# Optimization experiments

Measured on AMD Instinct MI355X. Metric: run time of the kernel, lower is better.

Reference implementation:

```python
import jax, jax.numpy as jnp
import numpy as np

B, SD, SE = 4, 2048, 2048
HID, HID_ = 300, 512
N_HEADS = 8


def setup_inputs() -> dict:
    key = jax.random.key(0)
    ks = jax.random.split(key, 7)
    en = jax.random.normal(ks[0], (B, SE, HID), dtype=jnp.float32)
    de = jax.random.normal(ks[1], (B, SD, HID), dtype=jnp.float32)
    mask = jax.random.randint(ks[2], (1, 1, SD, SE), 0, 2).astype(jnp.bool_)
    WQ = jax.random.normal(ks[3], (HID, HID_), dtype=jnp.float32)
    WK = jax.random.normal(ks[4], (HID, HID_), dtype=jnp.float32)
    WV = jax.random.normal(ks[5], (HID, HID_), dtype=jnp.float32)
    WO = jax.random.normal(ks[6], (HID_, HID), dtype=jnp.float32)
    return {"en": en, "de": de, "mask": mask, "WQ": WQ, "WK": WK, "WV": WV, "WO": WO}


def reference(en, de, mask, WQ, WK, WV, WO):
    # Faithful to the torch module (dropout in eval mode => identity).
    d_k = de.shape[-1]  # NOTE: original scales by sqrt(hidden_dim)=sqrt(300), not head_dim
    b_d, s_d = de.shape[0], de.shape[1]
    b_e, s_e = en.shape[0], en.shape[1]
    # head axis is the LAST axis of the reshape (size 8), exactly as the original view/permute
    q = jnp.transpose((de @ WQ).reshape(b_d, s_d, -1, N_HEADS), (3, 0, 1, 2))  # [8,B,Sd,64]
    k = jnp.transpose((en @ WK).reshape(b_e, s_e, -1, N_HEADS), (3, 0, 2, 1))  # [8,B,64,Se]
    v = jnp.transpose((en @ WV).reshape(b_e, s_e, -1, N_HEADS), (3, 0, 1, 2))  # [8,B,Se,64]
    e = jnp.matmul(q, k) / jnp.sqrt(jnp.asarray(d_k, dtype=q.dtype))           # [8,B,Sd,Se]
    e = jnp.where(mask, jnp.asarray(-1e9, dtype=e.dtype), e)
    alpha = jax.nn.softmax(e, axis=3)
    head3 = jnp.matmul(alpha, v)                                               # [8,B,Sd,64]
    # torch.cat((head3[0],...,head3[7]), 2) == move head axis into feature concat order
    a = jnp.concatenate([head3[h] for h in range(N_HEADS)], axis=2)            # [B,Sd,512]
    return a @ WO                                                              # [B,Sd,300]
```

## Files before the change

### kernel.cpp

```cpp
#include <hip/hip_runtime.h>
#include <hip/hip_bf16.h>
#include <math.h>

#define B_      4
#define SD_     2048
#define SE_     2048
#define HIDIN   300
#define HIDMID  512
#define NH      8
#define DH      64
#define ESZ     ((size_t)4194304)
#define BUFB    24576

typedef __attribute__((ext_vector_type(8))) short          s16x8;
typedef __attribute__((ext_vector_type(8))) unsigned short u16x8;
typedef __attribute__((ext_vector_type(4))) unsigned short u16x4;
typedef __attribute__((ext_vector_type(4))) float          f32x4;

#define MFMA16 __builtin_amdgcn_mfma_f32_16x16x32_bf16

#define QSCALE  0.0832940411f
#define NEGL   -1.4426950e9f
#define DEFER_THR 24.0f

__device__ __forceinline__ unsigned short f2bf(float f) {
    unsigned int u = __float_as_uint(f);
    u += 0x7fffu + ((u >> 16) & 1u);
    return (unsigned short)(u >> 16);
}
__device__ __forceinline__ float bf2f(unsigned short s) {
    return __uint_as_float((unsigned int)s << 16);
}
__device__ __forceinline__ void gload16(const void* g, void* l) {
    __builtin_amdgcn_global_load_lds(
        (const __attribute__((address_space(1))) void*)g,
        (__attribute__((address_space(3))) void*)l, 16, 0, 0);
}
__device__ __forceinline__ float fexp2(float x) {
#if __has_builtin(__builtin_amdgcn_exp2f)
    return __builtin_amdgcn_exp2f(x);
#else
    return exp2f(x);
#endif
}

#define OF_QH   ((size_t)0)
#define OF_QL   (ESZ)
#define OF_KH   (2*ESZ)
#define OF_KL   (3*ESZ)
#define OF_VT   (4*ESZ)
#define OF_CA   (5*ESZ)
#define OF_CW   (OF_CA + 10485760)
#define OF_WOT  (OF_CW + 983040)

__global__ __launch_bounds__(256) void bias_kernel(const int* __restrict__ mask,
                                                   unsigned int* __restrict__ BiasT)
{
    const int idx = blockIdx.x * 256 + threadIdx.x;
    const int q = idx >> 5, tile = idx & 31;
    const int* __restrict__ mrow = mask + (size_t)q * SE_ + tile * 64;
    const unsigned int NEGB = (unsigned int)f2bf(NEGL);
    const int qblk = q >> 4, qlo = q & 15;
#pragma unroll
    for (int g = 0; g < 4; ++g) {
        unsigned int w[8];
#pragma unroll
        for (int sub = 0; sub < 4; ++sub) {
            const int4 mm = *(const int4*)(mrow + sub * 16 + g * 4);
            w[sub * 2]     = (mm.x ? NEGB : 0u) | ((mm.y ? NEGB : 0u) << 16);
            w[sub * 2 + 1] = (mm.z ? NEGB : 0u) | ((mm.w ? NEGB : 0u) << 16);
        }
        unsigned int* dst = BiasT +
            ((((size_t)qblk * 32 + tile) * 4 + g) * 16 + qlo) * 8;
        *(uint4*)dst       = make_uint4(w[0], w[1], w[2], w[3]);
        *(uint4*)(dst + 4) = make_uint4(w[4], w[5], w[6], w[7]);
    }
}

__global__ __launch_bounds__(256) void convA_kernel(
    const float* __restrict__ de, const float* __restrict__ en,
    unsigned short* __restrict__ CA)
{
    const int idx = blockIdx.x * 256 + threadIdx.x;
    const int mat = blockIdx.y;
    const float* __restrict__ A = mat ? en : de;
    unsigned short* __restrict__ H = CA + (size_t)mat * 5242880;
    unsigned short* __restrict__ L = H + 2621440;
    const int row = idx / 10, ch = idx - row * 10;
    float v[32];
    if (ch < 9) {
#pragma unroll
        for (int i = 0; i < 8; ++i) {
            const float4 f = *(const float4*)(A + (size_t)row * 300 + ch * 32 + i * 4);
            v[i*4+0] = f.x; v[i*4+1] = f.y; v[i*4+2] = f.z; v[i*4+3] = f.w;
        }
    } else {
#pragma unroll
        for (int i = 0; i < 32; ++i) {
            const int k = 288 + i;
            v[i] = (k < 300) ? A[(size_t)row * 300 + k] : 0.f;
        }
    }
    const int r128 = row & 127;
    const int xr = (r128 >> 1) & 3;
    const size_t tb = ((size_t)(row >> 7) * 10 + ch) * 4096 + r128 * 32;
#pragma unroll
    for (int sub = 0; sub < 4; ++sub) {
        const int slot = sub ^ xr;
        u16x8 hv, lv;
#pragma unroll
        for (int e = 0; e < 8; ++e) {
            const float f = v[sub * 8 + e];
            const unsigned short h = f2bf(f);
            hv[e] = h; lv[e] = f2bf(f - bf2f(h));
        }
        *(u16x8*)(H + tb + slot * 8) = hv;
        *(u16x8*)(L + tb + slot * 8) = lv;
    }
}

__global__ __launch_bounds__(256) void convW_kernel(
    const float* __restrict__ WQ, const float* __restrict__ WK,
    const float* __restrict__ WV, const float* __restrict__ WO,
    unsigned short* __restrict__ CW, unsigned short* __restrict__ WOT)
{
    const int idx = blockIdx.x * 256 + threadIdx.x;
    if (idx < 122880) {
        const int which = idx / 40960;
        const int rem = idx - which * 40960;
        const int k = rem >> 7;
        const int n0 = (rem & 127) * 4;
        const float* __restrict__ W = which == 0 ? WQ : (which == 1 ? WK : WV);
        unsigned short* __restrict__ H = CW + (size_t)which * 327680;
        unsigned short* __restrict__ L = H + 163840;
        const float sc = (which == 0) ? QSCALE : 1.f;
        float4 w = make_float4(0.f, 0.f, 0.f, 0.f);
        if (k < 300) w = *(const float4*)(W + (size_t)k * 512 + n0);
        const float wv4[4] = {w.x * sc, w.y * sc, w.z * sc, w.w * sc};
        const int ch = k >> 5, kk = k & 31;
#pragma unroll
        for (int j = 0; j < 4; ++j) {
            const int n = n0 + j, ntile = n >> 7, nr = n & 127;
            const size_t o = ((size_t)(ntile * 10 + ch) * 128 + nr) * 32
                           + (((kk >> 3) ^ ((nr >> 1) & 3)) << 3) + (kk & 7);
            const unsigned short h = f2bf(wv4[j]);
            H[o] = h;
            if (which < 2) L[o] = f2bf(wv4[j] - bf2f(h));
        }
    } else {
        const int idx2 = idx - 122880;
        const int k = idx2 / 96, n4 = idx2 - k * 96;
        const int n0 = n4 * 4;
        float4 w = make_float4(0.f, 0.f, 0.f, 0.f);
        if (n0 < 300) w = *(const float4*)(WO + (size_t)k * 300 + n0);
        const float wv4[4] = {w.x, w.y, w.z, w.w};
        const int ch = k >> 5, kk = k & 31;
#pragma unroll
        for (int j = 0; j < 4; ++j) {
            const int n = n0 + j, ntile = n >> 7, nr = n & 127;
            const size_t o = ((size_t)(ntile * 16 + ch) * 128 + nr) * 32
                           + (((kk >> 3) ^ ((nr >> 1) & 3)) << 3) + (kk & 7);
            WOT[o] = f2bf(wv4[j]);
        }
    }
}

__global__ __launch_bounds__(256) void proj_qk_kernel(
    const unsigned short* __restrict__ CA, const unsigned short* __restrict__ CW,
    unsigned short* __restrict__ Qh, unsigned short* __restrict__ Ql,
    unsigned short* __restrict__ KhT, unsigned short* __restrict__ KlT)
{
    const int lin = blockIdx.x;
    const int which = lin >> 8;
    const int t = lin & 255;
    const int stile = (t & 7) | ((t >> 5) << 3);
    const int jtile = (t >> 3) & 3;
    const int tid = threadIdx.x, wv = tid >> 6, lane = tid & 63;
    const int li = lane & 15, g = lane >> 4;
    const int wr = wv >> 1, wc = wv & 1;

    __shared__ __align__(16) char LBp[65536];

    const unsigned short* __restrict__ pAh =
        CA + (size_t)which * 5242880 + (size_t)stile * 40960 + tid * 8;
    const unsigned short* __restrict__ pAl = pAh + 2621440;
    const unsigned short* __restrict__ pWh =
        CW + (size_t)which * 327680 + (size_t)jtile * 40960 + tid * 8;
    const unsigned short* __restrict__ pWl = pWh + 163840;

#define STAGEP(ch, bofs) {                                                    \
        char* db = LBp + (bofs) + wv * 1024;                                  \
        const size_t co = (size_t)(ch) * 4096;                                \
        gload16(pAh + co,        db);                                         \
        gload16(pAh + co + 2048, db + 4096);                                  \
        gload16(pAl + co,        db + 8192);                                  \
        gload16(pAl + co + 2048, db + 12288);                                 \
        gload16(pWh + co,        db + 16384);                                 \
        gload16(pWh + co + 2048, db + 20480);                                 \
        gload16(pWl + co,        db + 24576);                                 \
        gload16(pWl + co + 2048, db + 28672);                                 \
    }

    int offA[4], offW[4];
#pragma unroll
    for (int ssub = 0; ssub < 4; ++ssub) {
        const int r = wr * 64 + ssub * 16 + li;
        offA[ssub] = r * 64 + ((g ^ ((r >> 1) & 3)) << 4);
    }
#pragma unroll
    for (int jsub = 0; jsub < 4; ++jsub) {
        const int n = wc * 64 + jsub * 16 + li;
        offW[jsub] = n * 64 + ((g ^ ((n >> 1) & 3)) << 4);
    }

    f32x4 acc[4][4];
#pragma unroll
    for (int i = 0; i < 4; ++i)
#pragma unroll
        for (int j = 0; j < 4; ++j) acc[i][j] = (f32x4){0.f, 0.f, 0.f, 0.f};

    STAGEP(0, 0)
    __syncthreads();

#pragma unroll 1
    for (int ch = 0; ch < 10; ++ch) {
        const int bofs = (ch & 1) * 32768;
        if (ch < 9) STAGEP(ch + 1, bofs ^ 32768)
        const char* bp = LBp + bofs;
        s16x8 ah[4], al[4], wh[4], wl[4];
#pragma unroll
        for (int ssub = 0; ssub < 4; ++ssub) {
            ah[ssub] = *(const s16x8*)(bp + offA[ssub]);
            al[ssub] = *(const s16x8*)(bp + 8192 + offA[ssub]);
        }
#pragma unroll
        for (int jsub = 0; jsub < 4; ++jsub) {
            wh[jsub] = *(const s16x8*)(bp + 16384 + offW[jsub]);
            wl[jsub] = *(const s16x8*)(bp + 24576 + offW[jsub]);
        }
        __builtin_amdgcn_s_setprio(1);
#pragma unroll
        for (int ssub = 0; ssub < 4; ++ssub)
#pragma unroll
            for (int jsub = 0; jsub < 4; ++jsub) {
                acc[ssub][jsub] = MFMA16(ah[ssub], wh[jsub], acc[ssub][jsub], 0, 0, 0);
                acc[ssub][jsub] = MFMA16(ah[ssub], wl[jsub], acc[ssub][jsub], 0, 0, 0);
                acc[ssub][jsub] = MFMA16(al[ssub], wh[jsub], acc[ssub][jsub], 0, 0, 0);
            }
        __builtin_amdgcn_s_setprio(0);
        __syncthreads();
    }
#undef STAGEP

    const int jgbase = jtile * 128 + wc * 64 + li;
    const int sbase0 = stile * 128 + wr * 64 + 4 * g;
#pragma unroll
    for (int jsub = 0; jsub < 4; ++jsub) {
        const int jgg = jgbase + jsub * 16;
        const int d = jgg >> 3, hh = jgg & 7;
#pragma unroll
        for (int ssub = 0; ssub < 4; ++ssub) {
            const f32x4 v = acc[ssub][jsub];
            const int sg0 = sbase0 + ssub * 16;
            const int bbv = sg0 >> 11;
            const int bhn = bbv * 8 + hh;
            const int sl0 = sg0 & 2047;
            if (which == 0) {
                const size_t o = ((size_t)bhn * 2048 + sl0) * 64 + d;
#pragma unroll
                for (int r = 0; r < 4; ++r) {
                    const float val = v[r];
                    const unsigned short hi = f2bf(val);
                    Qh[o + r * 64] = hi;
                    Ql[o + r * 64] = f2bf(val - bf2f(hi));
                }
            } else {
                const int tile = sl0 >> 6, tt0 = sl0 & 63;
                const size_t tb = ((size_t)(bhn * 32 + tile)) << 12;
#pragma unroll
                for (int r = 0; r < 4; ++r) {
                    const int tt = tt0 + r;
                    const size_t o = tb + tt * 64 + (((d >> 3) ^ (tt & 7)) << 3) + (d & 7);
                    const float val = v[r];
                    const unsigned short hi = f2bf(val);
                    KhT[o] = hi;
                    KlT[o] = f2bf(val - bf2f(hi));
                }
            }
        }
    }
}

__global__ __launch_bounds__(256) void proj_v_kernel(
    const unsigned short* __restrict__ CA, const unsigned short* __restrict__ CW,
    unsigned short* __restrict__ VtT)
{
    const int t = blockIdx.x;
    const int stile = (t & 7) | ((t >> 5) << 3);
    const int jtile = (t >> 3) & 3;
    const int tid = threadIdx.x, wv = tid >> 6, lane = tid & 63;
    const int li = lane & 15, g = lane >> 4;
    const int wr = wv >> 1, wc = wv & 1;

    __shared__ __align__(16) char LBv[32768];

    const unsigned short* __restrict__ pAh =
        CA + (size_t)1 * 5242880 + (size_t)stile * 40960 + tid * 8;
    const unsigned short* __restrict__ pWh =
        CW + (size_t)2 * 327680 + (size_t)jtile * 40960 + tid * 8;

#define STAGEV(ch, bofs) {                                                    \
        char* db = LBv + (bofs) + wv * 1024;                                  \
        const size_t co = (size_t)(ch) * 4096;                                \
        gload16(pAh + co,        db);                                         \
        gload16(pAh + co + 2048, db + 4096);                                  \
        gload16(pWh + co,        db + 8192);                                  \
        gload16(pWh + co + 2048, db + 12288);                                 \
    }

    int offA[4], offW[4];
#pragma unroll
    for (int ssub = 0; ssub < 4; ++ssub) {
        const int r = wr * 64 + ssub * 16 + li;
        offA[ssub] = r * 64 + ((g ^ ((r >> 1) & 3)) << 4);
    }
#pragma unroll
    for (int jsub = 0; jsub < 4; ++jsub) {
        const int n = wc * 64 + jsub * 16 + li;
        offW[jsub] = 8192 + n * 64 + ((g ^ ((n >> 1) & 3)) << 4);
    }

    f32x4 acc[4][4];
#pragma unroll
    for (int i = 0; i < 4; ++i)
#pragma unroll
        for (int j = 0; j < 4; ++j) acc[i][j] = (f32x4){0.f, 0.f, 0.f, 0.f};

    STAGEV(0, 0)
    __syncthreads();

#pragma unroll 1
    for (int ch = 0; ch < 10; ++ch) {
        const int bofs = (ch & 1) * 16384;
        if (ch < 9) STAGEV(ch + 1, bofs ^ 16384)
        const char* bp = LBv + bofs;
        s16x8 ah[4], wh[4];
#pragma unroll
        for (int ssub = 0; ssub < 4; ++ssub)
            ah[ssub] = *(const s16x8*)(bp + offA[ssub]);
#pragma unroll
        for (int jsub = 0; jsub < 4; ++jsub)
            wh[jsub] = *(const s16x8*)(bp + offW[jsub]);
        __builtin_amdgcn_s_setprio(1);
#pragma unroll
        for (int ssub = 0; ssub < 4; ++ssub)
#pragma unroll
            for (int jsub = 0; jsub < 4; ++jsub)
                acc[ssub][jsub] = MFMA16(ah[ssub], wh[jsub], acc[ssub][jsub], 0, 0, 0);
        __builtin_amdgcn_s_setprio(0);
        __syncthreads();
    }
#undef STAGEV

    const int jgbase = jtile * 128 + wc * 64 + li;
    const int sbase0 = stile * 128 + wr * 64 + 4 * g;
#pragma unroll
    for (int jsub = 0; jsub < 4; ++jsub) {
        const int jgg = jgbase + jsub * 16;
        const int d = jgg >> 3, hh = jgg & 7;
#pragma unroll
        for (int ssub = 0; ssub < 4; ++ssub) {
            const f32x4 v = acc[ssub][jsub];
            const int sg0 = sbase0 + ssub * 16;
            const int bbv = sg0 >> 11;
            const int bhn = bbv * 8 + hh;
            const int sl0 = sg0 & 2047;
            const int tile = sl0 >> 6, tin0 = sl0 & 63;
            const size_t tb = ((size_t)(bhn * 32 + tile)) << 12;
            const int blk = tin0 >> 5, gg2 = (tin0 >> 2) & 3, half = (tin0 >> 4) & 1;
            const size_t o = tb + (size_t)d * 64
                           + ((((blk << 2) | gg2) ^ (d & 7)) << 3) + half * 4;
            u16x4 pk;
#pragma unroll
            for (int r = 0; r < 4; ++r) pk[r] = f2bf(v[r]);
            *(u16x4*)(VtT + o) = pk;
        }
    }
}

__global__ __launch_bounds__(512, 4) void attn_mfma_kernel(
    const unsigned short* __restrict__ Qh, const unsigned short* __restrict__ Ql,
    const unsigned short* __restrict__ KhT, const unsigned short* __restrict__ KlT,
    const unsigned short* __restrict__ VtT, const unsigned int* __restrict__ BiasT,
    unsigned short* __restrict__ AOb)
{
    const int lin = blockIdx.x + 16 * blockIdx.y;
    const int qt = (lin >> 3) & 15;
    const int bh = (lin & 7) + ((lin >> 7) << 3);
    const int bb = bh >> 3, hh = bh & 7;
    const int tid = threadIdx.x;
    const int wv = tid >> 6, lane = tid & 63;
    const int g = lane >> 4, li = lane & 15;
    const int q = qt * 128 + wv * 16 + li;

    __shared__ __align__(16) char LB[3 * BUFB];

    const size_t qoff = ((size_t)bh * SD_ + q) * DH + 8 * g;
    const s16x8 qh0 = *(const s16x8*)(Qh + qoff);
    const s16x8 qh1 = *(const s16x8*)(Qh + qoff + 32);
    const s16x8 ql0 = *(const s16x8*)(Ql + qoff);
    const s16x8 ql1 = *(const s16x8*)(Ql + qoff + 32);

    const unsigned short* __restrict__ sKh = KhT + ((size_t)bh << 17) + tid * 8;
    const unsigned short* __restrict__ sKl = KlT + ((size_t)bh << 17) + tid * 8;
    const unsigned short* __restrict__ sVt = VtT + ((size_t)bh << 17) + tid * 8;

    const int base0 = li * 128 + ((g ^ (li & 7)) << 4);
    const int base1 = li * 128 + (((4 + g) ^ (li & 7)) << 4);

    const size_t bbase = (size_t)(qt * 8 + wv) * 16384 + g * 128 + li * 8;

#define BIASLOAD(T, RA, RB) {                                                 \
        const uint4* p = (const uint4*)(BiasT + bbase + (size_t)(T) * 512);   \
        RA = p[0]; RB = p[1];                                                 \
    }
#define STAGE(tile, boff)                                                     \
    {                                                                         \
        char* db = LB + (boff) + wv * 1024;                                   \
        const size_t toff = (size_t)(tile) << 12;                             \
        gload16(sKh + toff, db);                                              \
        gload16(sKl + toff, db + 8192);                                       \
        gload16(sVt + toff, db + 16384);                                      \
    }

    float m = -INFINITY;
    f32x4 O[4], lacc;
#pragma unroll
    for (int i = 0; i < 4; ++i) O[i] = (f32x4){0.f, 0.f, 0.f, 0.f};
    lacc = (f32x4){0.f, 0.f, 0.f, 0.f};

    s16x8 ones;
#pragma unroll
    for (int i = 0; i < 8; ++i) ones[i] = (short)0x3F80;

    uint4 cBA, cBB, nBA, nBB;

#define UNPK(W, S, sub, cbase)                                                \
        S[sub][cbase]     = __uint_as_float((W) << 16);                       \
        S[sub][cbase + 1] = __uint_as_float((W) & 0xFFFF0000u);

#define ITER(IT, CBA_, CBB_, NBA_, NBB_)                                      \
    {                                                                         \
        BIASLOAD(((IT) + 1) & 31, NBA_, NBB_)                                 \
        STAGE(((IT) + 2) & 31, cs)                                            \
        f32x4 s[4];                                                           \
        UNPK(CBA_.x, s, 0, 0) UNPK(CBA_.y, s, 0, 2)                           \
        UNPK(CBA_.z, s, 1, 0) UNPK(CBA_.w, s, 1, 2)                           \
        UNPK(CBB_.x, s, 2, 0) UNPK(CBB_.y, s, 2, 2)                           \
        UNPK(CBB_.z, s, 3, 0) UNPK(CBB_.w, s, 3, 2)                           \
        __builtin_amdgcn_s_setprio(1);                                        \
        _Pragma("unroll")                                                     \
        for (int sub = 0; sub < 4; ++sub) {                                   \
            const s16x8 kh0 = *(const s16x8*)(LB + cc + base0 + sub * 2048);  \
            const s16x8 kh1 = *(const s16x8*)(LB + cc + base1 + sub * 2048);  \
            const s16x8 kl0 = *(const s16x8*)(LB + cc + base0 + 8192 + sub * 2048); \
            const s16x8 kl1 = *(const s16x8*)(LB + cc + base1 + 8192 + sub * 2048); \
            s[sub] = MFMA16(kh0, qh0, s[sub], 0, 0, 0);                       \
            s[sub] = MFMA16(kh0, ql0, s[sub], 0, 0, 0);                       \
            s[sub] = MFMA16(kl0, qh0, s[sub], 0, 0, 0);                       \
            s[sub] = MFMA16(kh1, qh1, s[sub], 0, 0, 0);                       \
            s[sub] = MFMA16(kh1, ql1, s[sub], 0, 0, 0);                       \
            s[sub] = MFMA16(kl1, qh1, s[sub], 0, 0, 0);                       \
        }                                                                     \
        __builtin_amdgcn_s_setprio(0);                                        \
        float x0 = fmaxf(fmaxf(s[0][0], s[0][1]), s[0][2]);                   \
        float x1 = fmaxf(fmaxf(s[0][3], s[1][0]), s[1][1]);                   \
        float x2 = fmaxf(fmaxf(s[1][2], s[1][3]), s[2][0]);                   \
        float x3 = fmaxf(fmaxf(s[2][1], s[2][2]), s[2][3]);                   \
        float x4 = fmaxf(fmaxf(s[3][0], s[3][1]), s[3][2]);                   \
        float tmax = fmaxf(fmaxf(fmaxf(x0, x1), fmaxf(x2, x3)),               \
                           fmaxf(x4, s[3][3]));                               \
        if (!__all(tmax <= m + DEFER_THR)) {                                  \
            float r = fmaxf(tmax, __shfl_xor(tmax, 16));                      \
            r = fmaxf(r, __shfl_xor(r, 32));                                  \
            const float mn  = fmaxf(m, r);                                    \
            const float scl = fexp2(m - mn);                                  \
            m = mn;                                                           \
            _Pragma("unroll")                                                 \
            for (int i = 0; i < 4; ++i) O[i] *= scl;                          \
            lacc *= scl;                                                      \
        }                                                                     \
        _Pragma("unroll")                                                     \
        for (int sub = 0; sub < 4; ++sub)                                     \
            _Pragma("unroll")                                                 \
            for (int c = 0; c < 4; ++c)                                       \
                s[sub][c] = fexp2(s[sub][c] - m);                             \
        union { s16x8 v; unsigned int w[4]; } P0, P1;                         \
        asm("v_cvt_pk_bf16_f32 %0, %1, %2" : "=v"(P0.w[0]) : "v"(s[0][0]), "v"(s[0][1])); \
        asm("v_cvt_pk_bf16_f32 %0, %1, %2" : "=v"(P0.w[1]) : "v"(s[0][2]), "v"(s[0][3])); \
        asm("v_cvt_pk_bf16_f32 %0, %1, %2" : "=v"(P0.w[2]) : "v"(s[1][0]), "v"(s[1][1])); \
        asm("v_cvt_pk_bf16_f32 %0, %1, %2" : "=v"(P0.w[3]) : "v"(s[1][2]), "v"(s[1][3])); \
        asm("v_cvt_pk_bf16_f32 %0, %1, %2" : "=v"(P1.w[0]) : "v"(s[2][0]), "v"(s[2][1])); \
        asm("v_cvt_pk_bf16_f32 %0, %1, %2" : "=v"(P1.w[1]) : "v"(s[2][2]), "v"(s[2][3])); \
        asm("v_cvt_pk_bf16_f32 %0, %1, %2" : "=v"(P1.w[2]) : "v"(s[3][0]), "v"(s[3][1])); \
        asm("v_cvt_pk_bf16_f32 %0, %1, %2" : "=v"(P1.w[3]) : "v"(s[3][2]), "v"(s[3][3])); \
        __builtin_amdgcn_s_setprio(1);                                        \
        _Pragma("unroll")                                                     \
        for (int dsub = 0; dsub < 4; ++dsub) {                                \
            const s16x8 vf0 = *(const s16x8*)(LB + cc + base0 + 16384 + dsub * 2048); \
            const s16x8 vf1 = *(const s16x8*)(LB + cc + base1 + 16384 + dsub * 2048); \
            O[dsub] = MFMA16(vf0, P0.v, O[dsub], 0, 0, 0);                    \
            O[dsub] = MFMA16(vf1, P1.v, O[dsub], 0, 0, 0);                    \
        }                                                                     \
        lacc = MFMA16(ones, P0.v, lacc, 0, 0, 0);                             \
        lacc = MFMA16(ones, P1.v, lacc, 0, 0, 0);                             \
        __builtin_amdgcn_s_setprio(0);                                        \
        asm volatile("s_waitcnt vmcnt(3)" ::: "memory");                      \
        __builtin_amdgcn_s_barrier();                                         \
        __builtin_amdgcn_sched_barrier(0);                                    \
        cc += BUFB; if (cc == 3 * BUFB) cc = 0;                               \
        cs += BUFB; if (cs == 3 * BUFB) cs = 0;                               \
    }

    int cc = 0, cs = 2 * BUFB;

    BIASLOAD(0, cBA, cBB)
    STAGE(0, 0)
    STAGE(1, BUFB)
    asm volatile("s_waitcnt vmcnt(3)" ::: "memory");
    __builtin_amdgcn_s_barrier();
    __builtin_amdgcn_sched_barrier(0);

#pragma unroll 1
    for (int it = 0; it < 32; it += 2) {
        ITER(it,     cBA, cBB, nBA, nBB)
        ITER(it + 1, nBA, nBB, cBA, cBB)
    }

    const float rl = 1.f / lacc[0];
    const int row = bb * 2048 + q;
    const int r128 = row & 127;
    const int xr = (r128 >> 1) & 3;
    unsigned short* __restrict__ ab = AOb + ((size_t)(row >> 7)) * 65536
                                    + r128 * 32 + (g & 1) * 4;
#pragma unroll
    for (int dsub = 0; dsub < 4; ++dsub) {
        const f32x4 o = O[dsub] * rl;
        const int ch = hh * 2 + (dsub >> 1);
        const int slot = ((dsub & 1) * 2 + (g >> 1)) ^ xr;
        u16x4 pk;
#pragma unroll
        for (int c = 0; c < 4; ++c) pk[c] = f2bf(o[c]);
        *(u16x4*)(ab + (size_t)ch * 4096 + slot * 8) = pk;
    }
#undef STAGE
#undef BIASLOAD
#undef UNPK
#undef ITER
}

__global__ __launch_bounds__(256) void epi_mfma_kernel(
    const unsigned short* __restrict__ AOb, const unsigned short* __restrict__ WOT,
    float* __restrict__ out)
{
    const int stile = blockIdx.x, jtile = blockIdx.y;
    const int tid = threadIdx.x, wv = tid >> 6, lane = tid & 63;
    const int li = lane & 15, g = lane >> 4;

    __shared__ __align__(16) char LBe[24576];

    const unsigned short* __restrict__ pA =
        AOb + (size_t)(stile >> 1) * 65536 + (stile & 1) * 2048 + tid * 8;
    const unsigned short* __restrict__ pW = WOT + (size_t)jtile * 65536 + tid * 8;

#define STAGEE(ch, bofs) {                                                    \
        char* dbA = LBe + (bofs) + wv * 1024;                                 \
        const size_t co = (size_t)(ch) * 4096;                                \
        gload16(pA + co,        dbA);                                         \
        gload16(pW + co,        dbA + 4096);                                  \
        gload16(pW + co + 2048, dbA + 8192);                                  \
    }

    int offA[4], offW[2];
#pragma unroll
    for (int ssub = 0; ssub < 4; ++ssub) {
        const int r = ssub * 16 + li;
        offA[ssub] = r * 64 + ((g ^ ((r >> 1) & 3)) << 4);
    }
#pragma unroll
    for (int jsub = 0; jsub < 2; ++jsub) {
        const int n = wv * 32 + jsub * 16 + li;
        offW[jsub] = 4096 + n * 64 + ((g ^ ((n >> 1) & 3)) << 4);
    }

    f32x4 acc[4][2];
#pragma unroll
    for (int i = 0; i < 4; ++i)
#pragma unroll
        for (int j = 0; j < 2; ++j) acc[i][j] = (f32x4){0.f, 0.f, 0.f, 0.f};

    STAGEE(0, 0)
    __syncthreads();

#pragma unroll 1
    for (int ch = 0; ch < 16; ++ch) {
        const int bofs = (ch & 1) * 12288;
        if (ch < 15) STAGEE(ch + 1, bofs ^ 12288)
        const char* bp = LBe + bofs;
        s16x8 ah[4], wh[2];
#pragma unroll
        for (int ssub = 0; ssub < 4; ++ssub)
            ah[ssub] = *(const s16x8*)(bp + offA[ssub]);
#pragma unroll
        for (int jsub = 0; jsub < 2; ++jsub)
            wh[jsub] = *(const s16x8*)(bp + offW[jsub]);
        __builtin_amdgcn_s_setprio(1);
#pragma unroll
        for (int ssub = 0; ssub < 4; ++ssub)
#pragma unroll
            for (int jsub = 0; jsub < 2; ++jsub)
                acc[ssub][jsub] = MFMA16(ah[ssub], wh[jsub], acc[ssub][jsub], 0, 0, 0);
        __builtin_amdgcn_s_setprio(0);
        __syncthreads();
    }
#undef STAGEE

    const int nbase = jtile * 128 + wv * 32 + li;
    const int rbase = stile * 64 + 4 * g;
#pragma unroll
    for (int jsub = 0; jsub < 2; ++jsub) {
        const int o = nbase + jsub * 16;
        if (o < HIDIN) {
#pragma unroll
            for (int ssub = 0; ssub < 4; ++ssub) {
                const f32x4 v = acc[ssub][jsub];
                const int r0 = rbase + ssub * 16;
#pragma unroll
                for (int r = 0; r < 4; ++r)
                    out[(size_t)(r0 + r) * HIDIN + o] = v[r];
            }
        }
    }
}

extern "C" void kernel_launch(void* const* d_in, const int* in_sizes, int n_in,
                              void* d_out, int out_size, void* d_ws, size_t ws_size,
                              hipStream_t stream)
{
    const float* en  = (const float*)d_in[0];
    const float* de  = (const float*)d_in[1];
    const int*   mask = (const int*)d_in[2];
    const float* WQ  = (const float*)d_in[3];
    const float* WK  = (const float*)d_in[4];
    const float* WV  = (const float*)d_in[5];
    const float* WO  = (const float*)d_in[6];
    float* out = (float*)d_out;

    unsigned short* ws2 = (unsigned short*)d_ws;
    unsigned short* Qh  = ws2 + OF_QH;
    unsigned short* Ql  = ws2 + OF_QL;
    unsigned short* KhT = ws2 + OF_KH;
    unsigned short* KlT = ws2 + OF_KL;
    unsigned short* VtT = ws2 + OF_VT;
    unsigned short* CA  = ws2 + OF_CA;
    unsigned short* CW  = ws2 + OF_CW;
    unsigned short* WOT = ws2 + OF_WOT;
    unsigned short* AOb = CA;
    unsigned int*  BiasT = (unsigned int*)(CA + 4194304);

    convA_kernel<<<dim3(320, 2), 256, 0, stream>>>(de, en, CA);
    convW_kernel<<<dim3(672), 256, 0, stream>>>(WQ, WK, WV, WO, CW, WOT);
    proj_qk_kernel<<<dim3(512), 256, 0, stream>>>(CA, CW, Qh, Ql, KhT, KlT);
    proj_v_kernel<<<dim3(256), 256, 0, stream>>>(CA, CW, VtT);
    bias_kernel<<<dim3(256), 256, 0, stream>>>(mask, BiasT);
    attn_mfma_kernel<<<dim3(16, 32), 512, 0, stream>>>(Qh, Ql, KhT, KlT, VtT,
                                                       BiasT, AOb);
    epi_mfma_kernel<<<dim3(128, 3), 256, 0, stream>>>(AOb, WOT, out);
}
```

Before: 176.0 us.

## Switch attention kernel to 32x32x16 MFMA tiles with 4-wave blocks

Rewrites the attention kernel to use 32x32x16 bf16 MFMA instructions instead of 16x16x32. Each wave now handles 32 query rows, and blocks shrink from 8 to 4 waves. The bias and V-transpose layouts are rearranged to match the new accumulator fragment layout. The row sum, previously computed with an MFMA against a ones vector, is now a VALU tree reduction. The aim is to cut LDS fragment reads per FLOP and MFMA issue overhead, at the cost of more registers per wave and fewer waves per CU.

```diff
diff --git a/kernel.cpp b/kernel.cpp
--- a/kernel.cpp
+++ b/kernel.cpp
@@ -12,12 +12,14 @@
 #define ESZ     ((size_t)4194304)
 #define BUFB    24576
 
-typedef __attribute__((ext_vector_type(8))) short          s16x8;
-typedef __attribute__((ext_vector_type(8))) unsigned short u16x8;
-typedef __attribute__((ext_vector_type(4))) unsigned short u16x4;
-typedef __attribute__((ext_vector_type(4))) float          f32x4;
+typedef __attribute__((ext_vector_type(8)))  short          s16x8;
+typedef __attribute__((ext_vector_type(8)))  unsigned short u16x8;
+typedef __attribute__((ext_vector_type(4)))  unsigned short u16x4;
+typedef __attribute__((ext_vector_type(4)))  float          f32x4;
+typedef __attribute__((ext_vector_type(16))) float          f32x16;
 
 #define MFMA16 __builtin_amdgcn_mfma_f32_16x16x32_bf16
+#define MFMA32 __builtin_amdgcn_mfma_f32_32x32x16_bf16
 
 #define QSCALE  0.0832940411f
 #define NEGL   -1.4426950e9f
@@ -57,23 +59,31 @@
                                                    unsigned int* __restrict__ BiasT)
 {
     const int idx = blockIdx.x * 256 + threadIdx.x;
-    const int q = idx >> 5, tile = idx & 31;
-    const int* __restrict__ mrow = mask + (size_t)q * SE_ + tile * 64;
+    const int q = idx >> 5, t64 = idx & 31;
+    const int* __restrict__ mrow = mask + (size_t)q * SE_ + t64 * 64;
     const unsigned int NEGB = (unsigned int)f2bf(NEGL);
-    const int qblk = q >> 4, qlo = q & 15;
-#pragma unroll
-    for (int g = 0; g < 4; ++g) {
-        unsigned int w[8];
-#pragma unroll
-        for (int sub = 0; sub < 4; ++sub) {
-            const int4 mm = *(const int4*)(mrow + sub * 16 + g * 4);
-            w[sub * 2]     = (mm.x ? NEGB : 0u) | ((mm.y ? NEGB : 0u) << 16);
-            w[sub * 2 + 1] = (mm.z ? NEGB : 0u) | ((mm.w ? NEGB : 0u) << 16);
-        }
-        unsigned int* dst = BiasT +
-            ((((size_t)qblk * 32 + tile) * 4 + g) * 16 + qlo) * 8;
-        *(uint4*)dst       = make_uint4(w[0], w[1], w[2], w[3]);
-        *(uint4*)(dst + 4) = make_uint4(w[4], w[5], w[6], w[7]);
+    int mv[64];
+#pragma unroll
+    for (int i = 0; i < 16; ++i) {
+        const int4 mm = *(const int4*)(mrow + i * 4);
+        mv[i*4+0] = mm.x; mv[i*4+1] = mm.y; mv[i*4+2] = mm.z; mv[i*4+3] = mm.w;
+    }
+    uint4* __restrict__ dst4 = (uint4*)BiasT;
+    const size_t cbase = ((size_t)(q >> 5) * 32 + t64) * 4;
+#pragma unroll
+    for (int hi = 0; hi < 2; ++hi) {
+#pragma unroll
+        for (int L = 0; L < 4; ++L) {
+            unsigned int wd[4];
+#pragma unroll
+            for (int i = 0; i < 4; ++i) {
+                const int w = L * 4 + i;
+                const int t0 = (w >> 3) * 32 + 2 * (w & 1) + 8 * ((w & 7) >> 1) + 4 * hi;
+                wd[i] = (mv[t0] ? NEGB : 0u) | ((mv[t0 + 1] ? NEGB : 0u) << 16);
+            }
+            dst4[(cbase + L) * 64 + hi * 32 + (q & 31)] =
+                make_uint4(wd[0], wd[1], wd[2], wd[3]);
+        }
     }
 }
 
@@ -377,9 +387,9 @@
             const int sl0 = sg0 & 2047;
             const int tile = sl0 >> 6, tin0 = sl0 & 63;
             const size_t tb = ((size_t)(bhn * 32 + tile)) << 12;
-            const int blk = tin0 >> 5, gg2 = (tin0 >> 2) & 3, half = (tin0 >> 4) & 1;
-            const size_t o = tb + (size_t)d * 64
-                           + ((((blk << 2) | gg2) ^ (d & 7)) << 3) + half * 4;
+            const int s_pre = ((tin0 >> 4) << 1) | ((tin0 >> 2) & 1);
+            const int j0 = ((tin0 >> 3) & 1) * 4;
+            const size_t o = tb + (size_t)d * 64 + ((s_pre ^ (d & 7)) << 3) + j0;
             u16x4 pk;
 #pragma unroll
             for (int r = 0; r < 4; ++r) pk[r] = f2bf(v[r]);
@@ -388,7 +398,7 @@
     }
 }
 
-__global__ __launch_bounds__(512, 4) void attn_mfma_kernel(
+__global__ __launch_bounds__(256, 2) void attn32_kernel(
     const unsigned short* __restrict__ Qh, const unsigned short* __restrict__ Ql,
     const unsigned short* __restrict__ KhT, const unsigned short* __restrict__ KlT,
     const unsigned short* __restrict__ VtT, const unsigned int* __restrict__ BiasT,
@@ -400,122 +410,156 @@
     const int bb = bh >> 3, hh = bh & 7;
     const int tid = threadIdx.x;
     const int wv = tid >> 6, lane = tid & 63;
-    const int g = lane >> 4, li = lane & 15;
-    const int q = qt * 128 + wv * 16 + li;
+    const int hi = lane >> 5, l31 = lane & 31, l7 = lane & 7;
+    const int q = qt * 128 + wv * 32 + l31;
 
     __shared__ __align__(16) char LB[3 * BUFB];
 
-    const size_t qoff = ((size_t)bh * SD_ + q) * DH + 8 * g;
-    const s16x8 qh0 = *(const s16x8*)(Qh + qoff);
-    const s16x8 qh1 = *(const s16x8*)(Qh + qoff + 32);
-    const s16x8 ql0 = *(const s16x8*)(Ql + qoff);
-    const s16x8 ql1 = *(const s16x8*)(Ql + qoff + 32);
+    const size_t qoff = ((size_t)bh * SD_ + q) * DH + hi * 8;
+    s16x8 qh[4], ql[4];
+#pragma unroll
+    for (int c = 0; c < 4; ++c) {
+        qh[c] = *(const s16x8*)(Qh + qoff + c * 16);
+        ql[c] = *(const s16x8*)(Ql + qoff + c * 16);
+    }
 
     const unsigned short* __restrict__ sKh = KhT + ((size_t)bh << 17) + tid * 8;
     const unsigned short* __restrict__ sKl = KlT + ((size_t)bh << 17) + tid * 8;
     const unsigned short* __restrict__ sVt = VtT + ((size_t)bh << 17) + tid * 8;
 
-    const int base0 = li * 128 + ((g ^ (li & 7)) << 4);
-    const int base1 = li * 128 + (((4 + g) ^ (li & 7)) << 4);
-
-    const size_t bbase = (size_t)(qt * 8 + wv) * 16384 + g * 128 + li * 8;
-
-#define BIASLOAD(T, RA, RB) {                                                 \
-        const uint4* p = (const uint4*)(BiasT + bbase + (size_t)(T) * 512);   \
-        RA = p[0]; RB = p[1];                                                 \
+    int koff[4];
+#pragma unroll
+    for (int c = 0; c < 4; ++c)
+        koff[c] = l31 * 128 + (((2 * c + hi) ^ l7) << 4);
+
+    const int qg = q >> 5;
+    const size_t blane4 = (size_t)hi * 32 + l31;
+    const uint4* __restrict__ Bias4 = (const uint4*)BiasT;
+
+#define BIASLOAD(T, R0, R1, R2, R3) {                                         \
+        const size_t b4 = (((size_t)qg * 32 + (T)) * 4) * 64 + blane4;        \
+        R0 = Bias4[b4];        R1 = Bias4[b4 + 64];                           \
+        R2 = Bias4[b4 + 128];  R3 = Bias4[b4 + 192];                          \
     }
 #define STAGE(tile, boff)                                                     \
     {                                                                         \
         char* db = LB + (boff) + wv * 1024;                                   \
         const size_t toff = (size_t)(tile) << 12;                             \
-        gload16(sKh + toff, db);                                              \
-        gload16(sKl + toff, db + 8192);                                       \
-        gload16(sVt + toff, db + 16384);                                      \
-    }
-
-    float m = -INFINITY;
-    f32x4 O[4], lacc;
-#pragma unroll
-    for (int i = 0; i < 4; ++i) O[i] = (f32x4){0.f, 0.f, 0.f, 0.f};
-    lacc = (f32x4){0.f, 0.f, 0.f, 0.f};
-
-    s16x8 ones;
-#pragma unroll
-    for (int i = 0; i < 8; ++i) ones[i] = (short)0x3F80;
-
-    uint4 cBA, cBB, nBA, nBB;
-
-#define UNPK(W, S, sub, cbase)                                                \
-        S[sub][cbase]     = __uint_as_float((W) << 16);                       \
-        S[sub][cbase + 1] = __uint_as_float((W) & 0xFFFF0000u);
-
-#define ITER(IT, CBA_, CBB_, NBA_, NBB_)                                      \
+        gload16(sKh + toff,        db);                                       \
+        gload16(sKh + toff + 2048, db + 4096);                                \
+        gload16(sKl + toff,        db + 8192);                                \
+        gload16(sKl + toff + 2048, db + 12288);                               \
+        gload16(sVt + toff,        db + 16384);                               \
+        gload16(sVt + toff + 2048, db + 20480);                               \
+    }
+
+    float m = -INFINITY, lacc = 0.f;
+    f32x16 O0, O1;
+#pragma unroll
+    for (int i = 0; i < 16; ++i) { O0[i] = 0.f; O1[i] = 0.f; }
+
+    uint4 cB0, cB1, cB2, cB3, nB0, nB1, nB2, nB3;
+
+#define UNPKW(W, S, r)                                                        \
+        S[r]     = __uint_as_float((W) << 16);                                \
+        S[r + 1] = __uint_as_float((W) & 0xFFFF0000u);
+
+#define ITER(IT, C0_, C1_, C2_, C3_, N0_, N1_, N2_, N3_)                      \
     {                                                                         \
-        BIASLOAD(((IT) + 1) & 31, NBA_, NBB_)                                 \
+        BIASLOAD(((IT) + 1) & 31, N0_, N1_, N2_, N3_)                         \
         STAGE(((IT) + 2) & 31, cs)                                            \
-        f32x4 s[4];                                                           \
-        UNPK(CBA_.x, s, 0, 0) UNPK(CBA_.y, s, 0, 2)                           \
-        UNPK(CBA_.z, s, 1, 0) UNPK(CBA_.w, s, 1, 2)                           \
-        UNPK(CBB_.x, s, 2, 0) UNPK(CBB_.y, s, 2, 2)                           \
-        UNPK(CBB_.z, s, 3, 0) UNPK(CBB_.w, s, 3, 2)                           \
+        f32x16 sA, sB;                                                        \
+        UNPKW(C0_.x, sA, 0)  UNPKW(C0_.y, sA, 2)                              \
+        UNPKW(C0_.z, sA, 4)  UNPKW(C0_.w, sA, 6)                              \
+        UNPKW(C1_.x, sA, 8)  UNPKW(C1_.y, sA, 10)                             \
+        UNPKW(C1_.z, sA, 12) UNPKW(C1_.w, sA, 14)                             \
+        UNPKW(C2_.x, sB, 0)  UNPKW(C2_.y, sB, 2)                              \
+        UNPKW(C2_.z, sB, 4)  UNPKW(C2_.w, sB, 6)                              \
+        UNPKW(C3_.x, sB, 8)  UNPKW(C3_.y, sB, 10)                             \
+        UNPKW(C3_.z, sB, 12) UNPKW(C3_.w, sB, 14)                             \
         __builtin_amdgcn_s_setprio(1);                                        \
         _Pragma("unroll")                                                     \
-        for (int sub = 0; sub < 4; ++sub) {                                   \
-            const s16x8 kh0 = *(const s16x8*)(LB + cc + base0 + sub * 2048);  \
-            const s16x8 kh1 = *(const s16x8*)(LB + cc + base1 + sub * 2048);  \
-            const s16x8 kl0 = *(const s16x8*)(LB + cc + base0 + 8192 + sub * 2048); \
-            const s16x8 kl1 = *(const s16x8*)(LB + cc + base1 + 8192 + sub * 2048); \
-            s[sub] = MFMA16(kh0, qh0, s[sub], 0, 0, 0);                       \
-            s[sub] = MFMA16(kh0, ql0, s[sub], 0, 0, 0);                       \
-            s[sub] = MFMA16(kl0, qh0, s[sub], 0, 0, 0);                       \
-            s[sub] = MFMA16(kh1, qh1, s[sub], 0, 0, 0);                       \
-            s[sub] = MFMA16(kh1, ql1, s[sub], 0, 0, 0);                       \
-            s[sub] = MFMA16(kl1, qh1, s[sub], 0, 0, 0);                       \
+        for (int c = 0; c < 4; ++c) {                                         \
+            const s16x8 kh0 = *(const s16x8*)(LB + cc + koff[c]);             \
+            const s16x8 kh1 = *(const s16x8*)(LB + cc + 4096 + koff[c]);      \
+            const s16x8 kl0 = *(const s16x8*)(LB + cc + 8192 + koff[c]);      \
+            const s16x8 kl1 = *(const s16x8*)(LB + cc + 12288 + koff[c]);     \
+            sA = MFMA32(kh0, qh[c], sA, 0, 0, 0);                             \
+            sA = MFMA32(kh0, ql[c], sA, 0, 0, 0);                             \
+            sA = MFMA32(kl0, qh[c], sA, 0, 0, 0);                             \
+            sB = MFMA32(kh1, qh[c], sB, 0, 0, 0);                             \
+            sB = MFMA32(kh1, ql[c], sB, 0, 0, 0);                             \
+            sB = MFMA32(kl1, qh[c], sB, 0, 0, 0);                             \
         }                                                                     \
         __builtin_amdgcn_s_setprio(0);                                        \
-        float x0 = fmaxf(fmaxf(s[0][0], s[0][1]), s[0][2]);                   \
-        float x1 = fmaxf(fmaxf(s[0][3], s[1][0]), s[1][1]);                   \
-        float x2 = fmaxf(fmaxf(s[1][2], s[1][3]), s[2][0]);                   \
-        float x3 = fmaxf(fmaxf(s[2][1], s[2][2]), s[2][3]);                   \
-        float x4 = fmaxf(fmaxf(s[3][0], s[3][1]), s[3][2]);                   \
-        float tmax = fmaxf(fmaxf(fmaxf(x0, x1), fmaxf(x2, x3)),               \
-                           fmaxf(x4, s[3][3]));                               \
+        float tv[32];                                                         \
+        _Pragma("unroll")                                                     \
+        for (int i = 0; i < 16; ++i) { tv[i] = sA[i]; tv[16 + i] = sB[i]; }   \
+        _Pragma("unroll")                                                     \
+        for (int st = 16; st > 0; st >>= 1)                                   \
+            _Pragma("unroll")                                                 \
+            for (int i = 0; i < st; ++i) tv[i] = fmaxf(tv[i], tv[i + st]);    \
+        const float tmax = tv[0];                                             \
         if (!__all(tmax <= m + DEFER_THR)) {                                  \
-            float r = fmaxf(tmax, __shfl_xor(tmax, 16));                      \
-            r = fmaxf(r, __shfl_xor(r, 32));                                  \
+            float r = fmaxf(tmax, __shfl_xor(tmax, 32));                      \
             const float mn  = fmaxf(m, r);                                    \
             const float scl = fexp2(m - mn);                                  \
             m = mn;                                                           \
             _Pragma("unroll")                                                 \
-            for (int i = 0; i < 4; ++i) O[i] *= scl;                          \
+            for (int i = 0; i < 16; ++i) { O0[i] *= scl; O1[i] *= scl; }      \
             lacc *= scl;                                                      \
         }                                                                     \
         _Pragma("unroll")                                                     \
-        for (int sub = 0; sub < 4; ++sub)                                     \
+        for (int i = 0; i < 16; ++i) {                                        \
+            sA[i] = fexp2(sA[i] - m);                                         \
+            sB[i] = fexp2(sB[i] - m);                                         \
+        }                                                                     \
+        float sv[32];                                                         \
+        _Pragma("unroll")                                                     \
+        for (int i = 0; i < 16; ++i) { sv[i] = sA[i]; sv[16 + i] = sB[i]; }   \
+        _Pragma("unroll")                                                     \
+        for (int st = 16; st > 0; st >>= 1)                                   \
             _Pragma("unroll")                                                 \
-            for (int c = 0; c < 4; ++c)                                       \
-                s[sub][c] = fexp2(s[sub][c] - m);                             \
-        union { s16x8 v; unsigned int w[4]; } P0, P1;                         \
-        asm("v_cvt_pk_bf16_f32 %0, %1, %2" : "=v"(P0.w[0]) : "v"(s[0][0]), "v"(s[0][1])); \
-        asm("v_cvt_pk_bf16_f32 %0, %1, %2" : "=v"(P0.w[1]) : "v"(s[0][2]), "v"(s[0][3])); \
-        asm("v_cvt_pk_bf16_f32 %0, %1, %2" : "=v"(P0.w[2]) : "v"(s[1][0]), "v"(s[1][1])); \
-        asm("v_cvt_pk_bf16_f32 %0, %1, %2" : "=v"(P0.w[3]) : "v"(s[1][2]), "v"(s[1][3])); \
-        asm("v_cvt_pk_bf16_f32 %0, %1, %2" : "=v"(P1.w[0]) : "v"(s[2][0]), "v"(s[2][1])); \
-        asm("v_cvt_pk_bf16_f32 %0, %1, %2" : "=v"(P1.w[1]) : "v"(s[2][2]), "v"(s[2][3])); \
-        asm("v_cvt_pk_bf16_f32 %0, %1, %2" : "=v"(P1.w[2]) : "v"(s[3][0]), "v"(s[3][1])); \
-        asm("v_cvt_pk_bf16_f32 %0, %1, %2" : "=v"(P1.w[3]) : "v"(s[3][2]), "v"(s[3][3])); \
+            for (int i = 0; i < st; ++i) sv[i] += sv[i + st];                 \
+        lacc += sv[0];                                                        \
+        union { s16x8 v; unsigned int w[4]; } P0, P1, P2, P3;                 \
+        asm("v_cvt_pk_bf16_f32 %0, %1, %2" : "=v"(P0.w[0]) : "v"(sA[0]),  "v"(sA[1]));  \
+        asm("v_cvt_pk_bf16_f32 %0, %1, %2" : "=v"(P0.w[1]) : "v"(sA[2]),  "v"(sA[3]));  \
+        asm("v_cvt_pk_bf16_f32 %0, %1, %2" : "=v"(P0.w[2]) : "v"(sA[4]),  "v"(sA[5]));  \
+        asm("v_cvt_pk_bf16_f32 %0, %1, %2" : "=v"(P0.w[3]) : "v"(sA[6]),  "v"(sA[7]));  \
+        asm("v_cvt_pk_bf16_f32 %0, %1, %2" : "=v"(P1.w[0]) : "v"(sA[8]),  "v"(sA[9]));  \
+        asm("v_cvt_pk_bf16_f32 %0, %1, %2" : "=v"(P1.w[1]) : "v"(sA[10]), "v"(sA[11])); \
+        asm("v_cvt_pk_bf16_f32 %0, %1, %2" : "=v"(P1.w[2]) : "v"(sA[12]), "v"(sA[13])); \
+        asm("v_cvt_pk_bf16_f32 %0, %1, %2" : "=v"(P1.w[3]) : "v"(sA[14]), "v"(sA[15])); \
+        asm("v_cvt_pk_bf16_f32 %0, %1, %2" : "=v"(P2.w[0]) : "v"(sB[0]),  "v"(sB[1]));  \
+        asm("v_cvt_pk_bf16_f32 %0, %1, %2" : "=v"(P2.w[1]) : "v"(sB[2]),  "v"(sB[3]));  \
+        asm("v_cvt_pk_bf16_f32 %0, %1, %2" : "=v"(P2.w[2]) : "v"(sB[4]),  "v"(sB[5]));  \
+        asm("v_cvt_pk_bf16_f32 %0, %1, %2" : "=v"(P2.w[3]) : "v"(sB[6]),  "v"(sB[7]));  \
+        asm("v_cvt_pk_bf16_f32 %0, %1, %2" : "=v"(P3.w[0]) : "v"(sB[8]),  "v"(sB[9]));  \
+        asm("v_cvt_pk_bf16_f32 %0, %1, %2" : "=v"(P3.w[1]) : "v"(sB[10]), "v"(sB[11])); \
+        asm("v_cvt_pk_bf16_f32 %0, %1, %2" : "=v"(P3.w[2]) : "v"(sB[12]), "v"(sB[13])); \
+        asm("v_cvt_pk_bf16_f32 %0, %1, %2" : "=v"(P3.w[3]) : "v"(sB[14]), "v"(sB[15])); \
         __builtin_amdgcn_s_setprio(1);                                        \
-        _Pragma("unroll")                                                     \
-        for (int dsub = 0; dsub < 4; ++dsub) {                                \
-            const s16x8 vf0 = *(const s16x8*)(LB + cc + base0 + 16384 + dsub * 2048); \
-            const s16x8 vf1 = *(const s16x8*)(LB + cc + base1 + 16384 + dsub * 2048); \
-            O[dsub] = MFMA16(vf0, P0.v, O[dsub], 0, 0, 0);                    \
-            O[dsub] = MFMA16(vf1, P1.v, O[dsub], 0, 0, 0);                    \
+        {                                                                     \
+            const s16x8 v0 = *(const s16x8*)(LB + cc + 16384 + koff[0]);      \
+            const s16x8 v1 = *(const s16x8*)(LB + cc + 16384 + koff[1]);      \
+            const s16x8 v2 = *(const s16x8*)(LB + cc + 16384 + koff[2]);      \
+            const s16x8 v3 = *(const s16x8*)(LB + cc + 16384 + koff[3]);      \
+            O0 = MFMA32(v0, P0.v, O0, 0, 0, 0);                               \
+            O0 = MFMA32(v1, P1.v, O0, 0, 0, 0);                               \
+            O0 = MFMA32(v2, P2.v, O0, 0, 0, 0);                               \
+            O0 = MFMA32(v3, P3.v, O0, 0, 0, 0);                               \
+            const s16x8 w0 = *(const s16x8*)(LB + cc + 20480 + koff[0]);      \
+            const s16x8 w1 = *(const s16x8*)(LB + cc + 20480 + koff[1]);      \
+            const s16x8 w2 = *(const s16x8*)(LB + cc + 20480 + koff[2]);      \
+            const s16x8 w3 = *(const s16x8*)(LB + cc + 20480 + koff[3]);      \
+            O1 = MFMA32(w0, P0.v, O1, 0, 0, 0);                               \
+            O1 = MFMA32(w1, P1.v, O1, 0, 0, 0);                               \
+            O1 = MFMA32(w2, P2.v, O1, 0, 0, 0);                               \
+            O1 = MFMA32(w3, P3.v, O1, 0, 0, 0);                               \
         }                                                                     \
-        lacc = MFMA16(ones, P0.v, lacc, 0, 0, 0);                             \
-        lacc = MFMA16(ones, P1.v, lacc, 0, 0, 0);                             \
         __builtin_amdgcn_s_setprio(0);                                        \
-        asm volatile("s_waitcnt vmcnt(3)" ::: "memory");                      \
+        asm volatile("s_waitcnt vmcnt(6)" ::: "memory");                      \
         __builtin_amdgcn_s_barrier();                                         \
         __builtin_amdgcn_sched_barrier(0);                                    \
         cc += BUFB; if (cc == 3 * BUFB) cc = 0;                               \
@@ -524,38 +568,41 @@
 
     int cc = 0, cs = 2 * BUFB;
 
-    BIASLOAD(0, cBA, cBB)
+    BIASLOAD(0, cB0, cB1, cB2, cB3)
     STAGE(0, 0)
     STAGE(1, BUFB)
-    asm volatile("s_waitcnt vmcnt(3)" ::: "memory");
+    asm volatile("s_waitcnt vmcnt(6)" ::: "memory");
     __builtin_amdgcn_s_barrier();
     __builtin_amdgcn_sched_barrier(0);
 
 #pragma unroll 1
     for (int it = 0; it < 32; it += 2) {
-        ITER(it,     cBA, cBB, nBA, nBB)
-        ITER(it + 1, nBA, nBB, cBA, cBB)
-    }
-
-    const float rl = 1.f / lacc[0];
+        ITER(it,     cB0, cB1, cB2, cB3, nB0, nB1, nB2, nB3)
+        ITER(it + 1, nB0, nB1, nB2, nB3, cB0, cB1, cB2, cB3)
+    }
+
+    lacc += __shfl_xor(lacc, 32);
+    const float rl = 1.f / lacc;
     const int row = bb * 2048 + q;
     const int r128 = row & 127;
     const int xr = (r128 >> 1) & 3;
     unsigned short* __restrict__ ab = AOb + ((size_t)(row >> 7)) * 65536
-                                    + r128 * 32 + (g & 1) * 4;
-#pragma unroll
-    for (int dsub = 0; dsub < 4; ++dsub) {
-        const f32x4 o = O[dsub] * rl;
-        const int ch = hh * 2 + (dsub >> 1);
-        const int slot = ((dsub & 1) * 2 + (g >> 1)) ^ xr;
-        u16x4 pk;
-#pragma unroll
-        for (int c = 0; c < 4; ++c) pk[c] = f2bf(o[c]);
-        *(u16x4*)(ab + (size_t)ch * 4096 + slot * 8) = pk;
+                                    + r128 * 32 + 4 * hi;
+#pragma unroll
+    for (int dt = 0; dt < 2; ++dt) {
+        const int ch = hh * 2 + dt;
+#pragma unroll
+        for (int rg = 0; rg < 4; ++rg) {
+            u16x4 pk;
+#pragma unroll
+            for (int c = 0; c < 4; ++c)
+                pk[c] = f2bf((dt ? O1[4 * rg + c] : O0[4 * rg + c]) * rl);
+            *(u16x4*)(ab + (size_t)ch * 4096 + ((rg ^ xr) << 3)) = pk;
+        }
     }
 #undef STAGE
 #undef BIASLOAD
-#undef UNPK
+#undef UNPKW
 #undef ITER
 }
 
@@ -673,7 +720,7 @@
     proj_qk_kernel<<<dim3(512), 256, 0, stream>>>(CA, CW, Qh, Ql, KhT, KlT);
     proj_v_kernel<<<dim3(256), 256, 0, stream>>>(CA, CW, VtT);
     bias_kernel<<<dim3(256), 256, 0, stream>>>(mask, BiasT);
-    attn_mfma_kernel<<<dim3(16, 32), 512, 0, stream>>>(Qh, Ql, KhT, KlT, VtT,
-                                                       BiasT, AOb);
+    attn32_kernel<<<dim3(16, 32), 256, 0, stream>>>(Qh, Ql, KhT, KlT, VtT,
+                                                    BiasT, AOb);
     epi_mfma_kernel<<<dim3(128, 3), 256, 0, stream>>>(AOb, WOT, out);
 }
```

New measurement: 179.6 us. 1.02x slower.
